# Optimization experiments

Measured on AMD Instinct MI355X. Metric: run time of the kernel, lower is better.

Reference implementation:

```python
import math
import jax, jax.numpy as jnp
import numpy as np

H = 16  # num_heads
B, L, D = 1, 256, 1024


def setup_inputs() -> dict:
    key = jax.random.key(0)
    ks = jax.random.split(key, 12)
    s = 1.0 / math.sqrt(D)  # keep activations O(1)
    inp = {
        "mu": jax.random.normal(ks[0], (B, L, D), jnp.float32),
        "var": jax.random.uniform(ks[1], (B, L, D), jnp.float32) + 0.1,
    }
    names = ["q_mu", "q_var", "k_mu", "k_var", "v_mu", "v_var", "o_mu", "o_var"]
    for i, n in enumerate(names):
        inp["w" + n] = jax.random.normal(ks[2 + i], (D, D), jnp.float32) * s
        inp["b" + n] = jnp.zeros((D,), jnp.float32)
    return inp


def _split_heads(x):
    b, l, d = x.shape
    return x.reshape(b, l, H, d // H).transpose(0, 2, 1, 3)  # [B,H,L,Dh]


def _combine_heads(x):
    b, h, l, dh = x.shape
    return x.transpose(0, 2, 1, 3).reshape(b, l, h * dh)


def reference(mu, var, wq_mu, bq_mu, wq_var, bq_var, wk_mu, bk_mu, wk_var, bk_var,
              wv_mu, bv_mu, wv_var, bv_var, wo_mu, bo_mu, wo_var, bo_var):
    dk = mu.shape[-1] // H
    Qm = _split_heads(mu @ wq_mu + bq_mu)
    Qv = _split_heads(jax.nn.softplus(var @ wq_var + bq_var))
    Km = _split_heads(mu @ wk_mu + bk_mu)
    Kv = _split_heads(jax.nn.softplus(var @ wk_var + bk_var))
    Vm = _split_heads(mu @ wv_mu + bv_mu)
    Vv = _split_heads(jax.nn.softplus(var @ wv_var + bv_var))

    # per-element Gaussian KL, broadcast to [B,H,Lq,Lk,Dh] (as in the original)
    diff = (Qm[:, :, :, None, :] - Km[:, :, None, :, :]) ** 2
    ratio = Qv[:, :, :, None, :] / Kv[:, :, None, :, :]
    kl = diff / (2.0 * Kv[:, :, None, :, :]) + 0.5 * (ratio - jnp.log(ratio) - 1.0)
    scores = -kl.sum(-1) * (1.0 / math.sqrt(dk))  # [B,H,Lq,Lk]
    attn = jax.nn.softmax(scores, axis=-1)

    out_mu = jnp.einsum("bhqk,bhkd->bhqd", attn, Vm)
    out_var = jnp.einsum("bhqk,bhkd->bhqd", attn ** 2, Vv)

    O_mu = _combine_heads(out_mu)
    O_var = _combine_heads(out_var)
    mu_out = O_mu @ wo_mu + bo_mu
    var_out = jax.nn.softplus(O_var @ wo_var + bo_var)
    return mu_out, var_out
```

## Files before the change

### kernel.cpp

```cpp
#include <hip/hip_runtime.h>
#include <math.h>

typedef __bf16 bf16_t;
typedef bf16_t bf16x4 __attribute__((ext_vector_type(4)));
typedef bf16_t bf16x8 __attribute__((ext_vector_type(8)));
typedef float  f32x4  __attribute__((ext_vector_type(4)));

__device__ __forceinline__ float softplus_f(float x) {
    return (x > 20.f) ? x : log1pf(expf(x));
}

__device__ __forceinline__ float fast_rcp(float x) {
#if __has_builtin(__builtin_amdgcn_rcpf)
    return __builtin_amdgcn_rcpf(x);
#else
    return 1.0f / x;
#endif
}

struct PrepArgs { const float* src[8]; const float* mu; const float* var; };

__global__ __launch_bounds__(256) void prep_kernel(PrepArgs pa, bf16_t* __restrict__ wtbase,
                                                   bf16_t* __restrict__ dmu, bf16_t* __restrict__ dvar) {
    const int t = threadIdx.x;
    if (blockIdx.z == 8) {
        const int gid = (blockIdx.y * 16 + blockIdx.x) * 256 + t;
        const float* s; bf16_t* d; int off;
        if (gid < 32768) { s = pa.mu;  d = dmu;  off = gid * 8; }
        else             { s = pa.var; d = dvar; off = (gid - 32768) * 8; }
        float4 v0 = *(const float4*)(s + off);
        float4 v1 = *(const float4*)(s + off + 4);
        bf16x8 o;
        o[0] = (bf16_t)v0.x; o[1] = (bf16_t)v0.y; o[2] = (bf16_t)v0.z; o[3] = (bf16_t)v0.w;
        o[4] = (bf16_t)v1.x; o[5] = (bf16_t)v1.y; o[6] = (bf16_t)v1.z; o[7] = (bf16_t)v1.w;
        *(bf16x8*)(d + off) = o;
        return;
    }
    const int kt = blockIdx.x, nt = blockIdx.y, wm = blockIdx.z;
    const float* __restrict__ W = pa.src[wm];
    bf16_t* __restrict__ Wt = wtbase + (size_t)wm * 1048576;
    __shared__ bf16_t Ts[64][72];
    const int r0 = t >> 4, c4 = (t & 15) * 4;
#pragma unroll
    for (int rep = 0; rep < 4; ++rep) {
        const int r = r0 + rep * 16;
        const float4 v = *(const float4*)&W[(size_t)(kt * 64 + r) * 1024 + nt * 64 + c4];
        Ts[c4 + 0][r] = (bf16_t)v.x;
        Ts[c4 + 1][r] = (bf16_t)v.y;
        Ts[c4 + 2][r] = (bf16_t)v.z;
        Ts[c4 + 3][r] = (bf16_t)v.w;
    }
    __syncthreads();
#pragma unroll
    for (int rep = 0; rep < 2; ++rep) {
        const int chunk = t + rep * 256;
        const int n = chunk >> 3, kc = (chunk & 7) * 8;
        bf16x8 v = *(const bf16x8*)&Ts[n][kc];
        *(bf16x8*)&Wt[(size_t)(nt * 64 + n) * 1024 + kt * 64 + kc] = v;
    }
}

struct GemmArgs {
    const bf16_t* A[6];
    const bf16_t* Wt[6];
    const float*  bias[6];
    float*        dst[6];
    int           splus[6];
};

__global__ __launch_bounds__(256, 2) void gemm_splitk(GemmArgs args) {
    const int z = blockIdx.z;
    const bf16_t* __restrict__ A    = args.A[z];
    const bf16_t* __restrict__ Wt   = args.Wt[z];
    const float*  __restrict__ bias = args.bias[z];
    float*        __restrict__ dst  = args.dst[z];
    const int sp = args.splus[z];

    const int n_base = blockIdx.x * 64;
    const int m_base = blockIdx.y * 64;

    __shared__ __align__(16) unsigned char smem_raw[73728];
    bf16_t* stage = (bf16_t*)smem_raw;
    float*  Cr    = (float*)smem_raw;

    const int t = threadIdx.x;
    const int lane = t & 63;
    const int w = t >> 6;
    bf16_t* As = stage + w * 9216;
    bf16_t* Bs = As + 4608;

    const int r8 = lane >> 3, kb = lane & 7;
    const int fr = lane & 15, fq = lane >> 4, fk = fq * 8;

    f32x4 acc[4][4] = {};

#pragma unroll
    for (int s = 0; s < 4; ++s) {
        const int k0 = w * 256 + s * 64;
#pragma unroll
        for (int i = 0; i < 8; ++i) {
            const int row = i * 8 + r8;
            bf16x8 av = *(const bf16x8*)&A [(size_t)(m_base + row) * 1024 + k0 + kb * 8];
            bf16x8 bv = *(const bf16x8*)&Wt[(size_t)(n_base + row) * 1024 + k0 + kb * 8];
            *(bf16x8*)&As[row * 72 + kb * 8] = av;
            *(bf16x8*)&Bs[row * 72 + kb * 8] = bv;
        }
#pragma unroll
        for (int kh = 0; kh < 2; ++kh) {
            bf16x8 aF[4], bF[4];
#pragma unroll
            for (int i = 0; i < 4; ++i)
                aF[i] = *(const bf16x8*)&As[(i * 16 + fr) * 72 + kh * 32 + fk];
#pragma unroll
            for (int j = 0; j < 4; ++j)
                bF[j] = *(const bf16x8*)&Bs[(j * 16 + fr) * 72 + kh * 32 + fk];
#pragma unroll
            for (int i = 0; i < 4; ++i)
#pragma unroll
                for (int j = 0; j < 4; ++j)
                    acc[i][j] = __builtin_amdgcn_mfma_f32_16x16x32_bf16(aF[i], bF[j], acc[i][j], 0, 0, 0);
        }
    }

    __syncthreads();
    {
        float* Crw = Cr + w * 4352;
        const int orow = fq * 4;
#pragma unroll
        for (int i = 0; i < 4; ++i)
#pragma unroll
            for (int j = 0; j < 4; ++j)
#pragma unroll
                for (int rr = 0; rr < 4; ++rr)
                    Crw[(i * 16 + orow + rr) * 68 + j * 16 + fr] = acc[i][j][rr];
    }
    __syncthreads();

    const int cc = (t & 15) * 4;
    f32x4 bv4 = *(const f32x4*)&bias[n_base + cc];
#pragma unroll
    for (int i = 0; i < 4; ++i) {
        const int row = (t >> 4) + i * 16;
        f32x4 s0 = *(const f32x4*)&Cr[0 * 4352 + row * 68 + cc];
        f32x4 s1 = *(const f32x4*)&Cr[1 * 4352 + row * 68 + cc];
        f32x4 s2 = *(const f32x4*)&Cr[2 * 4352 + row * 68 + cc];
        f32x4 s3 = *(const f32x4*)&Cr[3 * 4352 + row * 68 + cc];
        f32x4 v = (s0 + s1) + (s2 + s3) + bv4;
        if (sp) {
            v[0] = softplus_f(v[0]); v[1] = softplus_f(v[1]);
            v[2] = softplus_f(v[2]); v[3] = softplus_f(v[3]);
        }
        *(f32x4*)&dst[(size_t)(m_base + row) * 1024 + n_base + cc] = v;
    }
}

__global__ __launch_bounds__(256) void feat_kernel(const float* __restrict__ Km,
                                                   const float* __restrict__ Kv,
                                                   bf16_t* __restrict__ Gbf,
                                                   float* __restrict__ cvec) {
    const int h = blockIdx.x, kb = blockIdx.y;
    const int t = threadIdx.x;
    const int kx = t & 63;
    const int dg = t >> 6;
    const int katt = kb * 64 + kx;
    const float* kvp = Kv + (size_t)katt * 1024 + h * 64 + dg * 16;
    const float* kmp = Km + (size_t)katt * 1024 + h * 64 + dg * 16;
    bf16_t* grow = Gbf + ((size_t)(h * 256 + katt)) * 128;
    float cp = 0.f;
#pragma unroll
    for (int c = 0; c < 4; ++c) {
        f32x4 kv = *(const f32x4*)(kvp + c * 4);
        f32x4 km = *(const f32x4*)(kmp + c * 4);
        bf16x4 o1, o2;
#pragma unroll
        for (int e = 0; e < 4; ++e) {
            const float r = 0.5f * fast_rcp(kv[e]);
            o1[e] = (bf16_t)r;
            o2[e] = (bf16_t)(-2.f * km[e] * r);
            cp += km[e] * km[e] * r + 0.5f * __logf(kv[e]);
        }
        *(bf16x4*)&grow[dg * 16 + c * 4]      = o1;
        *(bf16x4*)&grow[64 + dg * 16 + c * 4] = o2;
    }
    __shared__ float red[4][64];
    red[dg][kx] = cp;
    __syncthreads();
    if (dg == 0)
        cvec[h * 256 + katt] = red[0][kx] + red[1][kx] + red[2][kx] + red[3][kx];
}

#define OFF_VM   0
#define OFF_VV   36864
#define OFF_FS   73728
#define OFF_SC   82176
#define OFF_PHI  98816
#define OFF_PLO  107264
#define OFF_P2H  115712
#define OFF_P2L  124160
#define ATTN_SMEM 132608

__global__ __launch_bounds__(256) void attn_v6(const float* __restrict__ Qm,
                                               const float* __restrict__ Qv,
                                               const bf16_t* __restrict__ Gbf,
                                               const float* __restrict__ cvec,
                                               const float* __restrict__ Vm,
                                               const float* __restrict__ Vv,
                                               bf16_t* __restrict__ Omu,
                                               bf16_t* __restrict__ Ovar) {
    __shared__ __align__(16) unsigned char smem[ATTN_SMEM];
    bf16_t* Vsm = (bf16_t*)(smem + OFF_VM);
    bf16_t* Vsv = (bf16_t*)(smem + OFF_VV);
    float*  Fs  = (float*)(smem + OFF_FS);
    float*  Sc  = (float*)(smem + OFF_SC);
    bf16_t* Phi = (bf16_t*)(smem + OFF_PHI);
    bf16_t* Plo = (bf16_t*)(smem + OFF_PLO);
    bf16_t* P2h = (bf16_t*)(smem + OFF_P2H);
    bf16_t* P2l = (bf16_t*)(smem + OFF_P2L);

    const int qt = blockIdx.x, h = blockIdx.y;
    const int t = threadIdx.x, w = t >> 6, lane = t & 63;
    const int fr = lane & 15, fq = lane >> 4;
    const int n0 = w * 64;

    const bf16_t* gB = Gbf + ((size_t)(h * 256 + n0 + fr)) * 128 + fq * 8;

    bf16x8 bcur[4];
#pragma unroll
    for (int ks = 0; ks < 4; ++ks) bcur[ks] = *(const bf16x8*)(gB + ks * 32);

    {
        const int r = t >> 4, c = t & 15;
        f32x4 qm = *(const f32x4*)(Qm + (size_t)(qt * 16 + r) * 1024 + h * 64 + c * 4);
        f32x4 qv = *(const f32x4*)(Qv + (size_t)(qt * 16 + r) * 1024 + h * 64 + c * 4);
        *(f32x4*)&Fs[r * 132 + c * 4]      = qm * qm + qv;
        *(f32x4*)&Fs[r * 132 + 64 + c * 4] = qm;
    }
    __syncthreads();

    bf16x8 ahi[4], alo[4];
#pragma unroll
    for (int ks = 0; ks < 4; ++ks) {
        f32x4 f0 = *(const f32x4*)&Fs[fr * 132 + ks * 32 + fq * 8];
        f32x4 f1 = *(const f32x4*)&Fs[fr * 132 + ks * 32 + fq * 8 + 4];
#pragma unroll
        for (int e = 0; e < 4; ++e) {
            bf16_t hb = (bf16_t)f0[e];
            ahi[ks][e] = hb; alo[ks][e] = (bf16_t)(f0[e] - (float)hb);
            bf16_t hb2 = (bf16_t)f1[e];
            ahi[ks][e + 4] = hb2; alo[ks][e + 4] = (bf16_t)(f1[e] - (float)hb2);
        }
    }

    const int vk = t >> 2, vpart = t & 3;
#pragma unroll
    for (int nt = 0; nt < 4; ++nt) {
        const int ua = 2 * nt, ub = 2 * nt + 1;
        const float* vsa = ((ua >> 2) ? Vv : Vm) + (size_t)(vk + (ua & 3) * 64) * 1024 + h * 64 + vpart * 16;
        const float* vsb = ((ub >> 2) ? Vv : Vm) + (size_t)(vk + (ub & 3) * 64) * 1024 + h * 64 + vpart * 16;
        f32x4 va0 = *(const f32x4*)(vsa),     va1 = *(const f32x4*)(vsa + 4);
        f32x4 va2 = *(const f32x4*)(vsa + 8), va3 = *(const f32x4*)(vsa + 12);
        f32x4 vb0 = *(const f32x4*)(vsb),     vb1 = *(const f32x4*)(vsb + 4);
        f32x4 vb2 = *(const f32x4*)(vsb + 8), vb3 = *(const f32x4*)(vsb + 12);

        bf16x8 bnxt[4];
        if (nt < 3) {
#pragma unroll
            for (int ks = 0; ks < 4; ++ks)
                bnxt[ks] = *(const bf16x8*)(gB + (size_t)(nt + 1) * 2048 + ks * 32);
        }

        f32x4 acc = {0.f, 0.f, 0.f, 0.f};
#pragma unroll
        for (int ks = 0; ks < 4; ++ks) {
            acc = __builtin_amdgcn_mfma_f32_16x16x32_bf16(ahi[ks], bcur[ks], acc, 0, 0, 0);
            acc = __builtin_amdgcn_mfma_f32_16x16x32_bf16(alo[ks], bcur[ks], acc, 0, 0, 0);
        }

        {
            bf16_t* da = ((ua >> 2) ? Vsv : Vsm) + (vk + (ua & 3) * 64) * 72 + vpart * 16;
            bf16_t* db = ((ub >> 2) ? Vsv : Vsm) + (vk + (ub & 3) * 64) * 72 + vpart * 16;
            bf16x8 o0, o1;
            o0[0]=(bf16_t)va0[0]; o0[1]=(bf16_t)va0[1]; o0[2]=(bf16_t)va0[2]; o0[3]=(bf16_t)va0[3];
            o0[4]=(bf16_t)va1[0]; o0[5]=(bf16_t)va1[1]; o0[6]=(bf16_t)va1[2]; o0[7]=(bf16_t)va1[3];
            o1[0]=(bf16_t)va2[0]; o1[1]=(bf16_t)va2[1]; o1[2]=(bf16_t)va2[2]; o1[3]=(bf16_t)va2[3];
            o1[4]=(bf16_t)va3[0]; o1[5]=(bf16_t)va3[1]; o1[6]=(bf16_t)va3[2]; o1[7]=(bf16_t)va3[3];
            *(bf16x8*)(da)     = o0;
            *(bf16x8*)(da + 8) = o1;
            o0[0]=(bf16_t)vb0[0]; o0[1]=(bf16_t)vb0[1]; o0[2]=(bf16_t)vb0[2]; o0[3]=(bf16_t)vb0[3];
            o0[4]=(bf16_t)vb1[0]; o0[5]=(bf16_t)vb1[1]; o0[6]=(bf16_t)vb1[2]; o0[7]=(bf16_t)vb1[3];
            o1[0]=(bf16_t)vb2[0]; o1[1]=(bf16_t)vb2[1]; o1[2]=(bf16_t)vb2[2]; o1[3]=(bf16_t)vb2[3];
            o1[4]=(bf16_t)vb3[0]; o1[5]=(bf16_t)vb3[1]; o1[6]=(bf16_t)vb3[2]; o1[7]=(bf16_t)vb3[3];
            *(bf16x8*)(db)     = o0;
            *(bf16x8*)(db + 8) = o1;
        }

        const float cv = cvec[h * 256 + n0 + nt * 16 + fr];
        f32x4 lg = (acc + cv) * (-0.125f);
#pragma unroll
        for (int reg = 0; reg < 4; ++reg)
            Sc[(fq * 4 + reg) * 260 + n0 + nt * 16 + fr] = lg[reg];

#pragma unroll
        for (int ks = 0; ks < 4; ++ks) bcur[ks] = bnxt[ks];
    }
    __syncthreads();

    const int fw = w * 4;
    f32x4 sr[4];
#pragma unroll
    for (int r = 0; r < 4; ++r)
        sr[r] = *(const f32x4*)&Sc[(fw + r) * 260 + lane * 4];
#pragma unroll
    for (int r = 0; r < 4; ++r) {
        f32x4 s = sr[r];
        float mloc = fmaxf(fmaxf(s[0], s[1]), fmaxf(s[2], s[3]));
#pragma unroll
        for (int off = 32; off > 0; off >>= 1)
            mloc = fmaxf(mloc, __shfl_xor(mloc, off, 64));
        s[0] = __expf(s[0] - mloc); s[1] = __expf(s[1] - mloc);
        s[2] = __expf(s[2] - mloc); s[3] = __expf(s[3] - mloc);
        float sl = (s[0] + s[1]) + (s[2] + s[3]);
#pragma unroll
        for (int off = 32; off > 0; off >>= 1)
            sl += __shfl_xor(sl, off, 64);
        sr[r] = s * fast_rcp(sl);
    }

#pragma unroll
    for (int r = 0; r < 4; ++r) {
        bf16x4 phi, plo, p2hi, p2lo;
#pragma unroll
        for (int e = 0; e < 4; ++e) {
            const float p = sr[r][e];
            const bf16_t hb = (bf16_t)p;
            phi[e] = hb; plo[e] = (bf16_t)(p - (float)hb);
            const float p2 = p * p;
            const bf16_t h2 = (bf16_t)p2;
            p2hi[e] = h2; p2lo[e] = (bf16_t)(p2 - (float)h2);
        }
        const int row = fw + r;
        *(bf16x4*)&Phi[row * 264 + lane * 4] = phi;
        *(bf16x4*)&Plo[row * 264 + lane * 4] = plo;
        *(bf16x4*)&P2h[row * 264 + lane * 4] = p2hi;
        *(bf16x4*)&P2l[row * 264 + lane * 4] = p2lo;
    }
    __syncthreads();

    f32x4 accm = {0.f,0.f,0.f,0.f}, accv = {0.f,0.f,0.f,0.f};
#pragma unroll
    for (int k0 = 0; k0 < 256; k0 += 32) {
        const int ka = k0 + fq * 8;
        bf16x8 ahi2 = *(const bf16x8*)&Phi[fr * 264 + ka];
        bf16x8 alo2 = *(const bf16x8*)&Plo[fr * 264 + ka];
        bf16x8 a2h  = *(const bf16x8*)&P2h[fr * 264 + ka];
        bf16x8 a2l  = *(const bf16x8*)&P2l[fr * 264 + ka];
        bf16x8 bm, bv;
#pragma unroll
        for (int j = 0; j < 8; ++j) {
            const int kk = ka + j;
            bm[j] = Vsm[kk * 72 + w * 16 + fr];
            bv[j] = Vsv[kk * 72 + w * 16 + fr];
        }
        accm = __builtin_amdgcn_mfma_f32_16x16x32_bf16(ahi2, bm, accm, 0, 0, 0);
        accm = __builtin_amdgcn_mfma_f32_16x16x32_bf16(alo2, bm, accm, 0, 0, 0);
        accv = __builtin_amdgcn_mfma_f32_16x16x32_bf16(a2h,  bv, accv, 0, 0, 0);
        accv = __builtin_amdgcn_mfma_f32_16x16x32_bf16(a2l,  bv, accv, 0, 0, 0);
    }

#pragma unroll
    for (int reg = 0; reg < 4; ++reg) {
        const int qg = qt * 16 + fq * 4 + reg;
        const size_t ob = (size_t)qg * 1024 + h * 64 + w * 16 + fr;
        Omu[ob]  = (bf16_t)accm[reg];
        Ovar[ob] = (bf16_t)accv[reg];
    }
}

extern "C" void kernel_launch(void* const* d_in, const int* in_sizes, int n_in,
                              void* d_out, int out_size, void* d_ws, size_t ws_size,
                              hipStream_t stream) {
    const float* mu  = (const float*)d_in[0];
    const float* var = (const float*)d_in[1];

    uint8_t* ws = (uint8_t*)d_ws;
    bf16_t* Abf_mu  = (bf16_t*)(ws);
    bf16_t* Abf_var = (bf16_t*)(ws + (512u << 10));
    bf16_t* WtB     = (bf16_t*)(ws + (1u << 20));
    float*  Proj    = (float*)(ws + (17u << 20));
    bf16_t* Obf_mu  = (bf16_t*)(ws + (23u << 20));
    bf16_t* Obf_var = (bf16_t*)(ws + (23u << 20) + (512u << 10));
    bf16_t* Gbf     = (bf16_t*)(ws + (24u << 20));
    float*  cvec    = (float*)(ws + (25u << 20));

    PrepArgs pa;
    for (int i = 0; i < 8; ++i) pa.src[i] = (const float*)d_in[2 + 2 * i];
    pa.mu = mu; pa.var = var;
    prep_kernel<<<dim3(16, 16, 9), 256, 0, stream>>>(pa, WtB, Abf_mu, Abf_var);

    GemmArgs g1;
    for (int z = 0; z < 6; ++z) {
        g1.A[z]    = (z & 1) ? Abf_var : Abf_mu;
        g1.Wt[z]   = WtB + (size_t)z * 1048576;
        g1.bias[z] = (const float*)d_in[3 + 2 * z];
        g1.dst[z]  = Proj + (size_t)z * 262144;
        g1.splus[z] = (z & 1);
    }
    gemm_splitk<<<dim3(16, 4, 6), 256, 0, stream>>>(g1);

    feat_kernel<<<dim3(16, 4), 256, 0, stream>>>(Proj + 2 * 262144, Proj + 3 * 262144, Gbf, cvec);

    attn_v6<<<dim3(16, 16), 256, 0, stream>>>(Proj,
                                              Proj + 262144,
                                              Gbf, cvec,
                                              Proj + 4 * 262144,
                                              Proj + 5 * 262144,
                                              Obf_mu, Obf_var);

    GemmArgs g3;
    for (int z = 0; z < 6; ++z) {
        g3.A[z]    = Obf_mu;
        g3.Wt[z]   = WtB + (size_t)6 * 1048576;
        g3.bias[z] = (const float*)d_in[15];
        g3.dst[z]  = (float*)d_out;
        g3.splus[z] = 0;
    }
    g3.A[1]    = Obf_var;
    g3.Wt[1]   = WtB + (size_t)7 * 1048576;
    g3.bias[1] = (const float*)d_in[17];
    g3.dst[1]  = (float*)d_out + 262144;
    g3.splus[1] = 1;
    gemm_splitk<<<dim3(16, 4, 2), 256, 0, stream>>>(g3);
}
```

Before: 150.6 us.

## Fuse fp32-to-bf16 conversion and weight transpose into GEMM tile loads

Removes the separate prep kernel that converted activations and transposed and converted all eight weight matrices to bf16 in workspace. The GEMM now reads fp32 activations and row-major fp32 weights directly, converting to bf16 and transposing into shared memory while loading tiles. This drops one launch and the write-then-reread of the bf16 copies, but each GEMM block now loads twice the bytes for weights with strided float4 reads. The first-stage GEMM reads each input matrix several times across blocks.

```diff
diff --git a/kernel.cpp b/kernel.cpp
--- a/kernel.cpp
+++ b/kernel.cpp
@@ -18,63 +18,22 @@
 #endif
 }
 
-struct PrepArgs { const float* src[8]; const float* mu; const float* var; };
-
-__global__ __launch_bounds__(256) void prep_kernel(PrepArgs pa, bf16_t* __restrict__ wtbase,
-                                                   bf16_t* __restrict__ dmu, bf16_t* __restrict__ dvar) {
-    const int t = threadIdx.x;
-    if (blockIdx.z == 8) {
-        const int gid = (blockIdx.y * 16 + blockIdx.x) * 256 + t;
-        const float* s; bf16_t* d; int off;
-        if (gid < 32768) { s = pa.mu;  d = dmu;  off = gid * 8; }
-        else             { s = pa.var; d = dvar; off = (gid - 32768) * 8; }
-        float4 v0 = *(const float4*)(s + off);
-        float4 v1 = *(const float4*)(s + off + 4);
-        bf16x8 o;
-        o[0] = (bf16_t)v0.x; o[1] = (bf16_t)v0.y; o[2] = (bf16_t)v0.z; o[3] = (bf16_t)v0.w;
-        o[4] = (bf16_t)v1.x; o[5] = (bf16_t)v1.y; o[6] = (bf16_t)v1.z; o[7] = (bf16_t)v1.w;
-        *(bf16x8*)(d + off) = o;
-        return;
-    }
-    const int kt = blockIdx.x, nt = blockIdx.y, wm = blockIdx.z;
-    const float* __restrict__ W = pa.src[wm];
-    bf16_t* __restrict__ Wt = wtbase + (size_t)wm * 1048576;
-    __shared__ bf16_t Ts[64][72];
-    const int r0 = t >> 4, c4 = (t & 15) * 4;
-#pragma unroll
-    for (int rep = 0; rep < 4; ++rep) {
-        const int r = r0 + rep * 16;
-        const float4 v = *(const float4*)&W[(size_t)(kt * 64 + r) * 1024 + nt * 64 + c4];
-        Ts[c4 + 0][r] = (bf16_t)v.x;
-        Ts[c4 + 1][r] = (bf16_t)v.y;
-        Ts[c4 + 2][r] = (bf16_t)v.z;
-        Ts[c4 + 3][r] = (bf16_t)v.w;
-    }
-    __syncthreads();
-#pragma unroll
-    for (int rep = 0; rep < 2; ++rep) {
-        const int chunk = t + rep * 256;
-        const int n = chunk >> 3, kc = (chunk & 7) * 8;
-        bf16x8 v = *(const bf16x8*)&Ts[n][kc];
-        *(bf16x8*)&Wt[(size_t)(nt * 64 + n) * 1024 + kt * 64 + kc] = v;
-    }
-}
-
 struct GemmArgs {
-    const bf16_t* A[6];
-    const bf16_t* Wt[6];
-    const float*  bias[6];
-    float*        dst[6];
-    int           splus[6];
+    const void*  A[6];
+    const float* W[6];
+    const float* bias[6];
+    float*       dst[6];
+    int          splus[6];
+    int          afp32[6];
 };
 
 __global__ __launch_bounds__(256, 2) void gemm_splitk(GemmArgs args) {
     const int z = blockIdx.z;
-    const bf16_t* __restrict__ A    = args.A[z];
-    const bf16_t* __restrict__ Wt   = args.Wt[z];
-    const float*  __restrict__ bias = args.bias[z];
-    float*        __restrict__ dst  = args.dst[z];
+    const float* __restrict__ Wf   = args.W[z];
+    const float* __restrict__ bias = args.bias[z];
+    float*       __restrict__ dst  = args.dst[z];
     const int sp = args.splus[z];
+    const int af = args.afp32[z];
 
     const int n_base = blockIdx.x * 64;
     const int m_base = blockIdx.y * 64;
@@ -90,6 +49,7 @@
     bf16_t* Bs = As + 4608;
 
     const int r8 = lane >> 3, kb = lane & 7;
+    const int nq = lane & 15, kg = lane >> 4;
     const int fr = lane & 15, fq = lane >> 4, fk = fq * 8;
 
     f32x4 acc[4][4] = {};
@@ -97,13 +57,42 @@
 #pragma unroll
     for (int s = 0; s < 4; ++s) {
         const int k0 = w * 256 + s * 64;
-#pragma unroll
-        for (int i = 0; i < 8; ++i) {
-            const int row = i * 8 + r8;
-            bf16x8 av = *(const bf16x8*)&A [(size_t)(m_base + row) * 1024 + k0 + kb * 8];
-            bf16x8 bv = *(const bf16x8*)&Wt[(size_t)(n_base + row) * 1024 + k0 + kb * 8];
-            *(bf16x8*)&As[row * 72 + kb * 8] = av;
-            *(bf16x8*)&Bs[row * 72 + kb * 8] = bv;
+        if (af) {
+            const float* Af = (const float*)args.A[z];
+#pragma unroll
+            for (int i = 0; i < 8; ++i) {
+                const int row = i * 8 + r8;
+                const float* src = Af + (size_t)(m_base + row) * 1024 + k0 + kb * 8;
+                f32x4 v0 = *(const f32x4*)src;
+                f32x4 v1 = *(const f32x4*)(src + 4);
+                bf16x8 o;
+                o[0] = (bf16_t)v0[0]; o[1] = (bf16_t)v0[1]; o[2] = (bf16_t)v0[2]; o[3] = (bf16_t)v0[3];
+                o[4] = (bf16_t)v1[0]; o[5] = (bf16_t)v1[1]; o[6] = (bf16_t)v1[2]; o[7] = (bf16_t)v1[3];
+                *(bf16x8*)&As[row * 72 + kb * 8] = o;
+            }
+        } else {
+            const bf16_t* Ab = (const bf16_t*)args.A[z];
+#pragma unroll
+            for (int i = 0; i < 8; ++i) {
+                const int row = i * 8 + r8;
+                bf16x8 av = *(const bf16x8*)&Ab[(size_t)(m_base + row) * 1024 + k0 + kb * 8];
+                *(bf16x8*)&As[row * 72 + kb * 8] = av;
+            }
+        }
+#pragma unroll
+        for (int sub = 0; sub < 2; ++sub) {
+            f32x4 v[8];
+#pragma unroll
+            for (int j = 0; j < 8; ++j)
+                v[j] = *(const f32x4*)&Wf[(size_t)(k0 + kg * 16 + sub * 8 + j) * 1024 + n_base + nq * 4];
+#pragma unroll
+            for (int ii = 0; ii < 4; ++ii) {
+                const int e = (kg + ii) & 3;
+                bf16x8 o;
+#pragma unroll
+                for (int j = 0; j < 8; ++j) o[j] = (bf16_t)v[j][e];
+                *(bf16x8*)&Bs[(nq * 4 + e) * 72 + kg * 16 + sub * 8] = o;
+            }
         }
 #pragma unroll
         for (int kh = 0; kh < 2; ++kh) {
@@ -383,27 +372,20 @@
     const float* var = (const float*)d_in[1];
 
     uint8_t* ws = (uint8_t*)d_ws;
-    bf16_t* Abf_mu  = (bf16_t*)(ws);
-    bf16_t* Abf_var = (bf16_t*)(ws + (512u << 10));
-    bf16_t* WtB     = (bf16_t*)(ws + (1u << 20));
     float*  Proj    = (float*)(ws + (17u << 20));
     bf16_t* Obf_mu  = (bf16_t*)(ws + (23u << 20));
     bf16_t* Obf_var = (bf16_t*)(ws + (23u << 20) + (512u << 10));
     bf16_t* Gbf     = (bf16_t*)(ws + (24u << 20));
     float*  cvec    = (float*)(ws + (25u << 20));
 
-    PrepArgs pa;
-    for (int i = 0; i < 8; ++i) pa.src[i] = (const float*)d_in[2 + 2 * i];
-    pa.mu = mu; pa.var = var;
-    prep_kernel<<<dim3(16, 16, 9), 256, 0, stream>>>(pa, WtB, Abf_mu, Abf_var);
-
     GemmArgs g1;
     for (int z = 0; z < 6; ++z) {
-        g1.A[z]    = (z & 1) ? Abf_var : Abf_mu;
-        g1.Wt[z]   = WtB + (size_t)z * 1048576;
-        g1.bias[z] = (const float*)d_in[3 + 2 * z];
-        g1.dst[z]  = Proj + (size_t)z * 262144;
+        g1.A[z]     = (z & 1) ? (const void*)var : (const void*)mu;
+        g1.W[z]     = (const float*)d_in[2 + 2 * z];
+        g1.bias[z]  = (const float*)d_in[3 + 2 * z];
+        g1.dst[z]   = Proj + (size_t)z * 262144;
         g1.splus[z] = (z & 1);
+        g1.afp32[z] = 1;
     }
     gemm_splitk<<<dim3(16, 4, 6), 256, 0, stream>>>(g1);
 
@@ -418,14 +400,15 @@
 
     GemmArgs g3;
     for (int z = 0; z < 6; ++z) {
-        g3.A[z]    = Obf_mu;
-        g3.Wt[z]   = WtB + (size_t)6 * 1048576;
-        g3.bias[z] = (const float*)d_in[15];
-        g3.dst[z]  = (float*)d_out;
+        g3.A[z]     = (const void*)Obf_mu;
+        g3.W[z]     = (const float*)d_in[14];
+        g3.bias[z]  = (const float*)d_in[15];
+        g3.dst[z]   = (float*)d_out;
         g3.splus[z] = 0;
-    }
-    g3.A[1]    = Obf_var;
-    g3.Wt[1]   = WtB + (size_t)7 * 1048576;
+        g3.afp32[z] = 0;
+    }
+    g3.A[1]    = (const void*)Obf_var;
+    g3.W[1]    = (const float*)d_in[16];
     g3.bias[1] = (const float*)d_in[17];
     g3.dst[1]  = (float*)d_out + 262144;
     g3.splus[1] = 1;
```

Result: no change. 152.5 us (+1.2%).

## Double attention block to 512 threads and register-prefetch split-K GEMM tiles

Applied to the files above, without the earlier changes.

The attention kernel now launches 512 threads per block instead of 256. Each wave handles half as many score columns, softmax rows and V-loading rows, and the final PV product is split so separate waves compute the mu and var outputs. In the projection GEMM, global loads for the next k-slice are issued into registers before the current slice's MFMAs, so load latency can overlap with compute. The cost is more registers for prefetch buffers and a larger block that may lower occupancy, since the attention kernel already uses about 130KB of LDS.

```diff
diff --git a/kernel.cpp b/kernel.cpp
--- a/kernel.cpp
+++ b/kernel.cpp
@@ -92,18 +92,32 @@
     const int r8 = lane >> 3, kb = lane & 7;
     const int fr = lane & 15, fq = lane >> 4, fk = fq * 8;
 
+    const bf16_t* Ab = A  + (size_t)m_base * 1024 + w * 256 + kb * 8;
+    const bf16_t* Bb = Wt + (size_t)n_base * 1024 + w * 256 + kb * 8;
+
     f32x4 acc[4][4] = {};
 
+    bf16x8 pa[8], pb[8];
+#pragma unroll
+    for (int i = 0; i < 8; ++i) {
+        pa[i] = *(const bf16x8*)(Ab + (size_t)(i * 8 + r8) * 1024);
+        pb[i] = *(const bf16x8*)(Bb + (size_t)(i * 8 + r8) * 1024);
+    }
+
 #pragma unroll
     for (int s = 0; s < 4; ++s) {
-        const int k0 = w * 256 + s * 64;
 #pragma unroll
         for (int i = 0; i < 8; ++i) {
-            const int row = i * 8 + r8;
-            bf16x8 av = *(const bf16x8*)&A [(size_t)(m_base + row) * 1024 + k0 + kb * 8];
-            bf16x8 bv = *(const bf16x8*)&Wt[(size_t)(n_base + row) * 1024 + k0 + kb * 8];
-            *(bf16x8*)&As[row * 72 + kb * 8] = av;
-            *(bf16x8*)&Bs[row * 72 + kb * 8] = bv;
+            *(bf16x8*)&As[(i * 8 + r8) * 72 + kb * 8] = pa[i];
+            *(bf16x8*)&Bs[(i * 8 + r8) * 72 + kb * 8] = pb[i];
+        }
+        if (s < 3) {
+            const int off = (s + 1) * 64;
+#pragma unroll
+            for (int i = 0; i < 8; ++i) {
+                pa[i] = *(const bf16x8*)(Ab + (size_t)(i * 8 + r8) * 1024 + off);
+                pb[i] = *(const bf16x8*)(Bb + (size_t)(i * 8 + r8) * 1024 + off);
+            }
         }
 #pragma unroll
         for (int kh = 0; kh < 2; ++kh) {
@@ -199,7 +213,7 @@
 #define OFF_P2L  124160
 #define ATTN_SMEM 132608
 
-__global__ __launch_bounds__(256) void attn_v6(const float* __restrict__ Qm,
+__global__ __launch_bounds__(512) void attn_v7(const float* __restrict__ Qm,
                                                const float* __restrict__ Qv,
                                                const bf16_t* __restrict__ Gbf,
                                                const float* __restrict__ cvec,
@@ -220,7 +234,7 @@
     const int qt = blockIdx.x, h = blockIdx.y;
     const int t = threadIdx.x, w = t >> 6, lane = t & 63;
     const int fr = lane & 15, fq = lane >> 4;
-    const int n0 = w * 64;
+    const int n0 = w * 32;
 
     const bf16_t* gB = Gbf + ((size_t)(h * 256 + n0 + fr)) * 128 + fq * 8;
 
@@ -228,7 +242,7 @@
 #pragma unroll
     for (int ks = 0; ks < 4; ++ks) bcur[ks] = *(const bf16x8*)(gB + ks * 32);
 
-    {
+    if (t < 256) {
         const int r = t >> 4, c = t & 15;
         f32x4 qm = *(const f32x4*)(Qm + (size_t)(qt * 16 + r) * 1024 + h * 64 + c * 4);
         f32x4 qv = *(const f32x4*)(Qv + (size_t)(qt * 16 + r) * 1024 + h * 64 + c * 4);
@@ -251,22 +265,27 @@
         }
     }
 
-    const int vk = t >> 2, vpart = t & 3;
-#pragma unroll
-    for (int nt = 0; nt < 4; ++nt) {
-        const int ua = 2 * nt, ub = 2 * nt + 1;
-        const float* vsa = ((ua >> 2) ? Vv : Vm) + (size_t)(vk + (ua & 3) * 64) * 1024 + h * 64 + vpart * 16;
-        const float* vsb = ((ub >> 2) ? Vv : Vm) + (size_t)(vk + (ub & 3) * 64) * 1024 + h * 64 + vpart * 16;
+    const int tm = t & 255;
+    const int vk = tm >> 2, vpart = tm & 3;
+    const float* Vsrc = (t >= 256) ? Vv : Vm;
+    bf16_t*      Vdst = (t >= 256) ? Vsv : Vsm;
+
+#pragma unroll
+    for (int nt = 0; nt < 2; ++nt) {
+        const int ra = vk + (2 * nt) * 64;
+        const int rb = vk + (2 * nt + 1) * 64;
+        const float* vsa = Vsrc + (size_t)ra * 1024 + h * 64 + vpart * 16;
+        const float* vsb = Vsrc + (size_t)rb * 1024 + h * 64 + vpart * 16;
         f32x4 va0 = *(const f32x4*)(vsa),     va1 = *(const f32x4*)(vsa + 4);
         f32x4 va2 = *(const f32x4*)(vsa + 8), va3 = *(const f32x4*)(vsa + 12);
         f32x4 vb0 = *(const f32x4*)(vsb),     vb1 = *(const f32x4*)(vsb + 4);
         f32x4 vb2 = *(const f32x4*)(vsb + 8), vb3 = *(const f32x4*)(vsb + 12);
 
         bf16x8 bnxt[4];
-        if (nt < 3) {
+        if (nt < 1) {
 #pragma unroll
             for (int ks = 0; ks < 4; ++ks)
-                bnxt[ks] = *(const bf16x8*)(gB + (size_t)(nt + 1) * 2048 + ks * 32);
+                bnxt[ks] = *(const bf16x8*)(gB + 2048 + ks * 32);
         }
 
         f32x4 acc = {0.f, 0.f, 0.f, 0.f};
@@ -277,8 +296,8 @@
         }
 
         {
-            bf16_t* da = ((ua >> 2) ? Vsv : Vsm) + (vk + (ua & 3) * 64) * 72 + vpart * 16;
-            bf16_t* db = ((ub >> 2) ? Vsv : Vsm) + (vk + (ub & 3) * 64) * 72 + vpart * 16;
+            bf16_t* da = Vdst + ra * 72 + vpart * 16;
+            bf16_t* db = Vdst + rb * 72 + vpart * 16;
             bf16x8 o0, o1;
             o0[0]=(bf16_t)va0[0]; o0[1]=(bf16_t)va0[1]; o0[2]=(bf16_t)va0[2]; o0[3]=(bf16_t)va0[3];
             o0[4]=(bf16_t)va1[0]; o0[5]=(bf16_t)va1[1]; o0[6]=(bf16_t)va1[2]; o0[7]=(bf16_t)va1[3];
@@ -305,13 +324,13 @@
     }
     __syncthreads();
 
-    const int fw = w * 4;
-    f32x4 sr[4];
-#pragma unroll
-    for (int r = 0; r < 4; ++r)
+    const int fw = w * 2;
+    f32x4 sr[2];
+#pragma unroll
+    for (int r = 0; r < 2; ++r)
         sr[r] = *(const f32x4*)&Sc[(fw + r) * 260 + lane * 4];
 #pragma unroll
-    for (int r = 0; r < 4; ++r) {
+    for (int r = 0; r < 2; ++r) {
         f32x4 s = sr[r];
         float mloc = fmaxf(fmaxf(s[0], s[1]), fmaxf(s[2], s[3]));
 #pragma unroll
@@ -327,7 +346,7 @@
     }
 
 #pragma unroll
-    for (int r = 0; r < 4; ++r) {
+    for (int r = 0; r < 2; ++r) {
         bf16x4 phi, plo, p2hi, p2lo;
 #pragma unroll
         for (int e = 0; e < 4; ++e) {
@@ -346,33 +365,31 @@
     }
     __syncthreads();
 
-    f32x4 accm = {0.f,0.f,0.f,0.f}, accv = {0.f,0.f,0.f,0.f};
+    const int tile = w & 3;
+    const int isvar = w >> 2;
+    const bf16_t* Pa = isvar ? P2h : Phi;
+    const bf16_t* Pb = isvar ? P2l : Plo;
+    const bf16_t* Vs = isvar ? Vsv : Vsm;
+    f32x4 accp = {0.f, 0.f, 0.f, 0.f};
 #pragma unroll
     for (int k0 = 0; k0 < 256; k0 += 32) {
         const int ka = k0 + fq * 8;
-        bf16x8 ahi2 = *(const bf16x8*)&Phi[fr * 264 + ka];
-        bf16x8 alo2 = *(const bf16x8*)&Plo[fr * 264 + ka];
-        bf16x8 a2h  = *(const bf16x8*)&P2h[fr * 264 + ka];
-        bf16x8 a2l  = *(const bf16x8*)&P2l[fr * 264 + ka];
-        bf16x8 bm, bv;
-#pragma unroll
-        for (int j = 0; j < 8; ++j) {
-            const int kk = ka + j;
-            bm[j] = Vsm[kk * 72 + w * 16 + fr];
-            bv[j] = Vsv[kk * 72 + w * 16 + fr];
-        }
-        accm = __builtin_amdgcn_mfma_f32_16x16x32_bf16(ahi2, bm, accm, 0, 0, 0);
-        accm = __builtin_amdgcn_mfma_f32_16x16x32_bf16(alo2, bm, accm, 0, 0, 0);
-        accv = __builtin_amdgcn_mfma_f32_16x16x32_bf16(a2h,  bv, accv, 0, 0, 0);
-        accv = __builtin_amdgcn_mfma_f32_16x16x32_bf16(a2l,  bv, accv, 0, 0, 0);
-    }
-
+        bf16x8 a1 = *(const bf16x8*)&Pa[fr * 264 + ka];
+        bf16x8 a2 = *(const bf16x8*)&Pb[fr * 264 + ka];
+        bf16x8 bfr;
+#pragma unroll
+        for (int j = 0; j < 8; ++j)
+            bfr[j] = Vs[(ka + j) * 72 + tile * 16 + fr];
+        accp = __builtin_amdgcn_mfma_f32_16x16x32_bf16(a1, bfr, accp, 0, 0, 0);
+        accp = __builtin_amdgcn_mfma_f32_16x16x32_bf16(a2, bfr, accp, 0, 0, 0);
+    }
+
+    bf16_t* Out = isvar ? Ovar : Omu;
 #pragma unroll
     for (int reg = 0; reg < 4; ++reg) {
         const int qg = qt * 16 + fq * 4 + reg;
-        const size_t ob = (size_t)qg * 1024 + h * 64 + w * 16 + fr;
-        Omu[ob]  = (bf16_t)accm[reg];
-        Ovar[ob] = (bf16_t)accv[reg];
+        const size_t ob = (size_t)qg * 1024 + h * 64 + tile * 16 + fr;
+        Out[ob] = (bf16_t)accp[reg];
     }
 }
 
@@ -409,7 +426,7 @@
 
     feat_kernel<<<dim3(16, 4), 256, 0, stream>>>(Proj + 2 * 262144, Proj + 3 * 262144, Gbf, cvec);
 
-    attn_v6<<<dim3(16, 16), 256, 0, stream>>>(Proj,
+    attn_v7<<<dim3(16, 16), 512, 0, stream>>>(Proj,
                                               Proj + 262144,
                                               Gbf, cvec,
                                               Proj + 4 * 262144,
```

New measurement: 148.9 us. About the same (-1.1%).
